# Kernel tuning notes

Hardware: AMD Instinct MI355X
Metric: run time of the kernel (lower is better)

## Reference

```python
import jax, jax.numpy as jnp
import numpy as np

E = 16          # expert_num
T = 8192        # token_num
H = 1024        # hidden_size
I = 4096        # intermediate_size
LN_EPS = 1e-12


def setup_inputs() -> dict:
    key = jax.random.key(0)
    ks = jax.random.split(key, 6)
    hidden_states = jax.random.normal(ks[0], (T, H), dtype=jnp.float32)
    perm = jax.random.permutation(ks[1], T).astype(jnp.int32)
    s1 = 1.0 / np.sqrt(H)
    s2 = 1.0 / np.sqrt(I)
    w1 = jax.random.uniform(ks[2], (E, I, H), jnp.float32, -s1, s1)
    b1 = jax.random.uniform(ks[3], (E, I), jnp.float32, -s1, s1)
    w2 = jax.random.uniform(ks[4], (E, H, I), jnp.float32, -s2, s2)
    b2 = jax.random.uniform(ks[5], (E, H), jnp.float32, -s2, s2)
    ln_gamma = jnp.ones((H,), jnp.float32)
    ln_beta = jnp.zeros((H,), jnp.float32)
    return {"hidden_states": hidden_states, "perm": perm, "w1": w1, "b1": b1,
            "w2": w2, "b2": b2, "ln_gamma": ln_gamma, "ln_beta": ln_beta}


def _layer_norm(x, gamma, beta, eps):
    mu = jnp.mean(x, axis=-1, keepdims=True)
    var = jnp.var(x, axis=-1, keepdims=True)
    return (x - mu) * jax.lax.rsqrt(var + eps) * gamma + beta


def reference(hidden_states, perm, w1, b1, w2, b2, ln_gamma, ln_beta):
    # dispatch: gather tokens by random permutation, group per expert
    xp = hidden_states[perm].reshape(E, T // E, H)            # [E, T/E, H]
    # grouped expert FFN (batched GEMM replaces the per-expert Python loop)
    h = jnp.einsum('eth,eih->eti', xp, w1) + b1[:, None, :]   # [E, T/E, I]
    h = jax.nn.gelu(h, approximate=False)
    o = jnp.einsum('eti,ehi->eth', h, w2) + b2[:, None, :]    # [E, T/E, H]
    # scatter-restore via inverse permutation
    restore = jnp.argsort(perm)
    o = o.reshape(T, H)[restore]
    # dropout is identity (p=0, eval); residual + LayerNorm
    return _layer_norm(o + hidden_states, ln_gamma, ln_beta, LN_EPS)
```

## Files before the change

### kernel.cpp

```cpp
#include <hip/hip_runtime.h>
#include <hip/hip_bf16.h>
#include <stdint.h>

#define E_NUM 16
#define T_NUM 8192
#define H_DIM 1024
#define I_DIM 4096
#define MPE   512

typedef __attribute__((ext_vector_type(8))) short short8;
typedef __attribute__((ext_vector_type(4))) float f32x4;
using bf16 = __hip_bfloat16;

typedef const __attribute__((address_space(1))) void GLV;
typedef __attribute__((address_space(3))) void LDSV;

__device__ __forceinline__ uint32_t pack2_bf16(float a, float b) {
  union { float f; uint32_t u; } ua, ub;
  ua.f = a; ub.f = b;
  uint32_t x = ua.u + (0x7FFFu + ((ua.u >> 16) & 1u));
  uint32_t y = ub.u + (0x7FFFu + ((ub.u >> 16) & 1u));
  return (x >> 16) | (y & 0xFFFF0000u);
}

__device__ __forceinline__ uint2 cvt4u(float4 a) {
  union { uint2 u; __hip_bfloat162 h[2]; } r;
  r.h[0] = __float22bfloat162_rn({a.x, a.y});
  r.h[1] = __float22bfloat162_rn({a.z, a.w});
  return r.u;
}

__device__ __forceinline__ float fast_gelu(float x) {
  const float p = x * fmaf(x * x, -0.0713548162726f, -1.59576912161f);
  return x * __builtin_amdgcn_rcpf(1.0f + __expf(p));
}

__global__ __launch_bounds__(256)
void gather_cast_kernel(const float* __restrict__ hs, const int* __restrict__ perm,
                        uint32_t* __restrict__ xp) {
  const int r = blockIdx.x;
  const int t = threadIdx.x;
  const int src = perm[r];
  float4 v = ((const float4*)(hs + (size_t)src * H_DIM))[t];
  uint2 o;
  o.x = pack2_bf16(v.x, v.y);
  o.y = pack2_bf16(v.z, v.w);
  ((uint2*)(xp + (size_t)r * (H_DIM / 2)))[t] = o;
}

template<int EPI, int KSPLIT, int N, int KFULL, int KLEN, int LOG_NBN>
__global__ __launch_bounds__(1024, 4)
void moe_gemm_kernel(const bf16* __restrict__ A, const float* __restrict__ Bw,
                     const float* __restrict__ bias, bf16* __restrict__ Hout,
                     float* __restrict__ Pout) {
  constexpr int NK = KLEN / 32;
  __shared__ bf16 As[2][512 * 32];
  __shared__ bf16 Bs[2][64 * 64];

  const int nwg = gridDim.x, qx = nwg >> 3, orig = blockIdx.x;
  const int wg = (orig & 7) * qx + (orig >> 3);
  const int bn   = wg & ((1 << LOG_NBN) - 1);
  const int rest = wg >> LOG_NBN;
  const int ks = (KSPLIT == 2) ? (rest & 1) : 0;
  const int e  = (KSPLIT == 2) ? (rest >> 1) : rest;
  const int K0 = ks * KLEN;

  const int tid = threadIdx.x;
  const int l = tid & 63;
  const int w = tid >> 6;
  const int wr = w >> 1, wc = w & 1;
  const int fr = l & 15, fq = l >> 4;
  const int rx = fr & 7;

  const bf16*  Ae = A  + (size_t)e * MPE * KFULL + K0;
  const float* Be = Bw + ((size_t)e * N + (size_t)bn * 128) * KFULL + K0;

  const int apq = tid >> 3;
  const int ag  = (tid & 7) ^ (apq & 7);
  const bf16* As0 = Ae + (size_t)(apq       + 256 * (ag >> 2)) * KFULL + (ag & 3) * 8;
  const bf16* As1 = Ae + (size_t)(apq + 128 + 256 * (ag >> 2)) * KFULL + (ag & 3) * 8;

  const int bc = tid >> 3, bsg = tid & 7;
  const float* Bsrc = Be + (size_t)bc * KFULL + bsg * 4;
  const int bp  = bc & 63;
  const int bwo = bp * 64 + (((((bc >> 6) << 2) | (bsg >> 1)) ^ (bp & 7)) << 3)
                + (bsg & 1) * 4;

  const int aso = (((((wr >> 2) << 2)) | fq) ^ rx) * 8;
  const int bro = fr * 64 + ((((wc << 2) | fq) ^ rx) << 3);

  f32x4 acc[4][4];
#pragma unroll
  for (int m = 0; m < 4; ++m)
#pragma unroll
    for (int n = 0; n < 4; ++n) acc[m][n] = (f32x4){0.f, 0.f, 0.f, 0.f};

  float4 breg;

#define ISSUE(buf, kt)                                                              \
  {                                                                                 \
    breg = *(const float4*)(Bsrc + (kt) * 32);                                      \
    __builtin_amdgcn_global_load_lds((GLV*)(As0 + (kt) * 32),                       \
                                     (LDSV*)&As[buf][tid * 8], 16, 0, 0);           \
    __builtin_amdgcn_global_load_lds((GLV*)(As1 + (kt) * 32),                       \
                                     (LDSV*)&As[buf][(1024 + tid) * 8], 16, 0, 0);  \
  }
#define WRITE_B(buf) { *(uint2*)&Bs[buf][bwo] = cvt4u(breg); }

  ISSUE(0, 0);
  asm volatile("s_waitcnt vmcnt(2)" ::: "memory");
  __builtin_amdgcn_sched_barrier(0);
  WRITE_B(0);
  asm volatile("s_waitcnt vmcnt(0) lgkmcnt(0)" ::: "memory");
  __builtin_amdgcn_sched_barrier(0);
  __builtin_amdgcn_s_barrier();
  __builtin_amdgcn_sched_barrier(0);

  for (int t = 0; t < NK; ++t) {
    const int cur = t & 1, nxt = cur ^ 1;
    const bool more = (t + 1) < NK;

    if (more) ISSUE(nxt, t + 1);

    short8 a8[4];
#pragma unroll
    for (int m = 0; m < 4; ++m)
      a8[m] = *(const short8*)&As[cur][((wr & 3) * 64 + m * 16 + fr) * 64 + aso];
    short8 b8[4];
#pragma unroll
    for (int n = 0; n < 4; ++n)
      b8[n] = *(const short8*)&Bs[cur][bro + n * 1024];
#pragma unroll
    for (int m = 0; m < 4; ++m)
#pragma unroll
      for (int n = 0; n < 4; ++n)
        acc[m][n] = __builtin_amdgcn_mfma_f32_16x16x32_bf16(a8[m], b8[n], acc[m][n], 0, 0, 0);

    if (more) {
      asm volatile("s_waitcnt vmcnt(2)" ::: "memory");
      __builtin_amdgcn_sched_barrier(0);
      WRITE_B(nxt);
      asm volatile("s_waitcnt vmcnt(0) lgkmcnt(0)" ::: "memory");
      __builtin_amdgcn_sched_barrier(0);
      __builtin_amdgcn_s_barrier();
      __builtin_amdgcn_sched_barrier(0);
    }
  }
#undef ISSUE
#undef WRITE_B
  __syncthreads();

  if (EPI == 1) {
    float bv[4];
#pragma unroll
    for (int n = 0; n < 4; ++n)
      bv[n] = bias[(size_t)e * N + bn * 128 + wc * 64 + n * 16 + fr];
    bf16* He = Hout + (size_t)e * MPE * N;

    bf16* Ls = &As[0][0];
#pragma unroll
    for (int P = 0; P < 2; ++P) {
      if ((wr >> 2) == P) {
        const int wrl = wr & 3;
#pragma unroll
        for (int m = 0; m < 4; ++m) {
#pragma unroll
          for (int j = 0; j < 4; ++j) {
            const int lr = wrl * 64 + m * 16 + fq * 4 + j;
#pragma unroll
            for (int n = 0; n < 4; ++n) {
              const int c = wc * 64 + n * 16 + fr;
              const int byteoff = lr * 256 + ((c * 2) ^ ((lr & 7) << 4));
              Ls[byteoff >> 1] = __float2bfloat16(fast_gelu(acc[m][n][j] + bv[n]));
            }
          }
        }
      }
      __syncthreads();
#pragma unroll
      for (int q = 0; q < 4; ++q) {
        const int o = (tid + q * 1024) * 16;
        const int lr = o >> 8;
        const int cb = o & 255;
        const int sb = lr * 256 + (cb ^ ((lr & 7) << 4));
        uint4 v = *(const uint4*)((const char*)Ls + sb);
        *(uint4*)&He[(size_t)(P * 256 + lr) * N + bn * 128 + (cb >> 1)] = v;
      }
      __syncthreads();
    }
  } else {
    float* Pd = Pout + (size_t)ks * T_NUM * H_DIM + (size_t)e * MPE * N;
#pragma unroll
    for (int m = 0; m < 4; ++m) {
#pragma unroll
      for (int j = 0; j < 4; ++j) {
        const int row = wr * 64 + m * 16 + fq * 4 + j;
#pragma unroll
        for (int n = 0; n < 4; ++n) {
          const int col = bn * 128 + wc * 64 + n * 16 + fr;
          Pd[(size_t)row * N + col] = acc[m][n][j];
        }
      }
    }
  }
}

__global__ __launch_bounds__(256)
void ln_resid2_kernel(float* __restrict__ out, const float* __restrict__ hs,
                      const float* __restrict__ p0, const float* __restrict__ p1,
                      const float* __restrict__ b2, const float* __restrict__ gamma,
                      const float* __restrict__ beta, const int* __restrict__ perm,
                      const int two) {
  const int r = blockIdx.x;
  const int t = threadIdx.x;
  const int e = r >> 9;
  const int drow = perm[r];
  float4 a = ((const float4*)(p0 + (size_t)r * H_DIM))[t];
  if (two) {
    float4 b = ((const float4*)(p1 + (size_t)r * H_DIM))[t];
    a.x += b.x; a.y += b.y; a.z += b.z; a.w += b.w;
  }
  float4 bb = ((const float4*)(b2 + (size_t)e * H_DIM))[t];
  float4 h  = ((const float4*)(hs + (size_t)drow * H_DIM))[t];
  float v0 = a.x + bb.x + h.x, v1 = a.y + bb.y + h.y;
  float v2 = a.z + bb.z + h.z, v3 = a.w + bb.w + h.w;
  float s  = v0 + v1 + v2 + v3;
  float sq = v0 * v0 + v1 * v1 + v2 * v2 + v3 * v3;
#pragma unroll
  for (int off = 32; off > 0; off >>= 1) {
    s  += __shfl_down(s, off);
    sq += __shfl_down(sq, off);
  }
  __shared__ float ss[4], ssq[4];
  const int wv = t >> 6;
  if ((t & 63) == 0) { ss[wv] = s; ssq[wv] = sq; }
  __syncthreads();
  s  = ss[0] + ss[1] + ss[2] + ss[3];
  sq = ssq[0] + ssq[1] + ssq[2] + ssq[3];
  const float mu  = s * (1.0f / (float)H_DIM);
  const float var = sq * (1.0f / (float)H_DIM) - mu * mu;
  const float rs  = rsqrtf(var + 1e-12f);
  float4 g = ((const float4*)gamma)[t];
  float4 b = ((const float4*)beta)[t];
  float4 rr;
  rr.x = (v0 - mu) * rs * g.x + b.x;
  rr.y = (v1 - mu) * rs * g.y + b.y;
  rr.z = (v2 - mu) * rs * g.z + b.z;
  rr.w = (v3 - mu) * rs * g.w + b.w;
  ((float4*)(out + (size_t)drow * H_DIM))[t] = rr;
}

extern "C" void kernel_launch(void* const* d_in, const int* in_sizes, int n_in,
                              void* d_out, int out_size, void* d_ws, size_t ws_size,
                              hipStream_t stream) {
  const float* hs    = (const float*)d_in[0];
  const int*   perm  = (const int*)d_in[1];
  const float* w1    = (const float*)d_in[2];
  const float* b1    = (const float*)d_in[3];
  const float* w2    = (const float*)d_in[4];
  const float* b2    = (const float*)d_in[5];
  const float* gamma = (const float*)d_in[6];
  const float* beta  = (const float*)d_in[7];
  float* out = (float*)d_out;

  const size_t xp_b   = (size_t)T_NUM * H_DIM * sizeof(bf16);
  const size_t hbuf_b = (size_t)T_NUM * I_DIM * sizeof(bf16);
  const size_t part_b = (size_t)T_NUM * H_DIM * sizeof(float);

  bf16*  xp   = (bf16*)d_ws;
  bf16*  hbuf = (bf16*)((char*)d_ws + xp_b);
  float* pbuf = (float*)((char*)d_ws + xp_b + hbuf_b);

  gather_cast_kernel<<<T_NUM, 256, 0, stream>>>(hs, perm, (uint32_t*)xp);

  moe_gemm_kernel<1, 1, I_DIM, H_DIM, H_DIM, 5>
      <<<512, 1024, 0, stream>>>(xp, w1, b1, hbuf, nullptr);

  if (ws_size >= xp_b + hbuf_b + 2 * part_b) {
    moe_gemm_kernel<0, 2, H_DIM, I_DIM, I_DIM / 2, 3>
        <<<256, 1024, 0, stream>>>(hbuf, w2, nullptr, nullptr, pbuf);
    ln_resid2_kernel<<<T_NUM, 256, 0, stream>>>(out, hs, pbuf, pbuf + (size_t)T_NUM * H_DIM,
                                                b2, gamma, beta, perm, 1);
  } else {
    moe_gemm_kernel<0, 1, H_DIM, I_DIM, I_DIM, 3>
        <<<128, 1024, 0, stream>>>(hbuf, w2, nullptr, nullptr, pbuf);
    ln_resid2_kernel<<<T_NUM, 256, 0, stream>>>(out, hs, pbuf, nullptr,
                                                b2, gamma, beta, perm, 0);
  }
}
```

Measured before the change: 293.8 us.

## Halve GEMM M-tile to 256 rows with 512-thread blocks

Splits each expert's 512-row M block into two 256-row tiles, so the grouped GEMMs use 512-thread workgroups and launch twice as many blocks. The A staging buffer shrinks and each thread now loads and converts eight fp32 weights per K-step instead of four. The aim is to cut per-workgroup LDS use and barrier cost and to raise parallelism and occupancy. In exchange, each fp32 weight tile is read and converted to bf16 twice as often, once per M half.

```diff
diff --git a/kernel.cpp b/kernel.cpp
--- a/kernel.cpp
+++ b/kernel.cpp
@@ -23,10 +23,12 @@
   return (x >> 16) | (y & 0xFFFF0000u);
 }
 
-__device__ __forceinline__ uint2 cvt4u(float4 a) {
-  union { uint2 u; __hip_bfloat162 h[2]; } r;
+__device__ __forceinline__ uint4 cvt8u(float4 a, float4 b) {
+  union { uint4 u; __hip_bfloat162 h[4]; } r;
   r.h[0] = __float22bfloat162_rn({a.x, a.y});
   r.h[1] = __float22bfloat162_rn({a.z, a.w});
+  r.h[2] = __float22bfloat162_rn({b.x, b.y});
+  r.h[3] = __float22bfloat162_rn({b.z, b.w});
   return r.u;
 }
 
@@ -49,18 +51,19 @@
 }
 
 template<int EPI, int KSPLIT, int N, int KFULL, int KLEN, int LOG_NBN>
-__global__ __launch_bounds__(1024, 4)
+__global__ __launch_bounds__(512, 2)
 void moe_gemm_kernel(const bf16* __restrict__ A, const float* __restrict__ Bw,
                      const float* __restrict__ bias, bf16* __restrict__ Hout,
                      float* __restrict__ Pout) {
   constexpr int NK = KLEN / 32;
-  __shared__ bf16 As[2][512 * 32];
+  __shared__ bf16 As[2][256 * 32];
   __shared__ bf16 Bs[2][64 * 64];
 
   const int nwg = gridDim.x, qx = nwg >> 3, orig = blockIdx.x;
   const int wg = (orig & 7) * qx + (orig >> 3);
-  const int bn   = wg & ((1 << LOG_NBN) - 1);
-  const int rest = wg >> LOG_NBN;
+  const int bm   = wg & 1;
+  const int bn   = (wg >> 1) & ((1 << LOG_NBN) - 1);
+  const int rest = wg >> (1 + LOG_NBN);
   const int ks = (KSPLIT == 2) ? (rest & 1) : 0;
   const int e  = (KSPLIT == 2) ? (rest >> 1) : rest;
   const int K0 = ks * KLEN;
@@ -72,21 +75,20 @@
   const int fr = l & 15, fq = l >> 4;
   const int rx = fr & 7;
 
-  const bf16*  Ae = A  + (size_t)e * MPE * KFULL + K0;
+  const bf16*  Ae = A  + ((size_t)e * MPE + (size_t)bm * 256) * KFULL + K0;
   const float* Be = Bw + ((size_t)e * N + (size_t)bn * 128) * KFULL + K0;
 
-  const int apq = tid >> 3;
-  const int ag  = (tid & 7) ^ (apq & 7);
-  const bf16* As0 = Ae + (size_t)(apq       + 256 * (ag >> 2)) * KFULL + (ag & 3) * 8;
-  const bf16* As1 = Ae + (size_t)(apq + 128 + 256 * (ag >> 2)) * KFULL + (ag & 3) * 8;
-
-  const int bc = tid >> 3, bsg = tid & 7;
-  const float* Bsrc = Be + (size_t)bc * KFULL + bsg * 4;
+  const int p0 = tid >> 3;
+  const int ga = (tid & 7) ^ (p0 & 7);
+  const bf16* As0 = Ae + (size_t)(p0      + 128 * (ga >> 2)) * KFULL + (ga & 3) * 8;
+  const bf16* As1 = Ae + (size_t)(p0 + 64 + 128 * (ga >> 2)) * KFULL + (ga & 3) * 8;
+
+  const int bc = tid >> 2, bsg = tid & 3;
+  const float* Bsrc = Be + (size_t)bc * KFULL + bsg * 8;
   const int bp  = bc & 63;
-  const int bwo = bp * 64 + (((((bc >> 6) << 2) | (bsg >> 1)) ^ (bp & 7)) << 3)
-                + (bsg & 1) * 4;
-
-  const int aso = (((((wr >> 2) << 2)) | fq) ^ rx) * 8;
+  const int bwo = bp * 64 + (((((bc >> 6) << 2) | bsg) ^ (bp & 7)) << 3);
+
+  const int aso = (((((wr >> 1) << 2)) | fq) ^ rx) * 8;
   const int bro = fr * 64 + ((((wc << 2) | fq) ^ rx) << 3);
 
   f32x4 acc[4][4];
@@ -95,17 +97,18 @@
 #pragma unroll
     for (int n = 0; n < 4; ++n) acc[m][n] = (f32x4){0.f, 0.f, 0.f, 0.f};
 
-  float4 breg;
+  float4 br0, br1;
 
 #define ISSUE(buf, kt)                                                              \
   {                                                                                 \
-    breg = *(const float4*)(Bsrc + (kt) * 32);                                      \
+    br0 = *(const float4*)(Bsrc + (kt) * 32);                                       \
+    br1 = *(const float4*)(Bsrc + (kt) * 32 + 4);                                   \
     __builtin_amdgcn_global_load_lds((GLV*)(As0 + (kt) * 32),                       \
                                      (LDSV*)&As[buf][tid * 8], 16, 0, 0);           \
     __builtin_amdgcn_global_load_lds((GLV*)(As1 + (kt) * 32),                       \
-                                     (LDSV*)&As[buf][(1024 + tid) * 8], 16, 0, 0);  \
-  }
-#define WRITE_B(buf) { *(uint2*)&Bs[buf][bwo] = cvt4u(breg); }
+                                     (LDSV*)&As[buf][(512 + tid) * 8], 16, 0, 0);   \
+  }
+#define WRITE_B(buf) { *(uint4*)&Bs[buf][bwo] = cvt8u(br0, br1); }
 
   ISSUE(0, 0);
   asm volatile("s_waitcnt vmcnt(2)" ::: "memory");
@@ -125,7 +128,7 @@
     short8 a8[4];
 #pragma unroll
     for (int m = 0; m < 4; ++m)
-      a8[m] = *(const short8*)&As[cur][((wr & 3) * 64 + m * 16 + fr) * 64 + aso];
+      a8[m] = *(const short8*)&As[cur][((wr & 1) * 64 + m * 16 + fr) * 64 + aso];
     short8 b8[4];
 #pragma unroll
     for (int n = 0; n < 4; ++n)
@@ -160,8 +163,8 @@
     bf16* Ls = &As[0][0];
 #pragma unroll
     for (int P = 0; P < 2; ++P) {
-      if ((wr >> 2) == P) {
-        const int wrl = wr & 3;
+      if ((wr >> 1) == P) {
+        const int wrl = wr & 1;
 #pragma unroll
         for (int m = 0; m < 4; ++m) {
 #pragma unroll
@@ -179,12 +182,12 @@
       __syncthreads();
 #pragma unroll
       for (int q = 0; q < 4; ++q) {
-        const int o = (tid + q * 1024) * 16;
+        const int o = (tid + q * 512) * 16;
         const int lr = o >> 8;
         const int cb = o & 255;
         const int sb = lr * 256 + (cb ^ ((lr & 7) << 4));
         uint4 v = *(const uint4*)((const char*)Ls + sb);
-        *(uint4*)&He[(size_t)(P * 256 + lr) * N + bn * 128 + (cb >> 1)] = v;
+        *(uint4*)&He[(size_t)(bm * 256 + P * 128 + lr) * N + bn * 128 + (cb >> 1)] = v;
       }
       __syncthreads();
     }
@@ -194,7 +197,7 @@
     for (int m = 0; m < 4; ++m) {
 #pragma unroll
       for (int j = 0; j < 4; ++j) {
-        const int row = wr * 64 + m * 16 + fq * 4 + j;
+        const int row = bm * 256 + wr * 64 + m * 16 + fq * 4 + j;
 #pragma unroll
         for (int n = 0; n < 4; ++n) {
           const int col = bn * 128 + wc * 64 + n * 16 + fr;
@@ -274,16 +277,16 @@
   gather_cast_kernel<<<T_NUM, 256, 0, stream>>>(hs, perm, (uint32_t*)xp);
 
   moe_gemm_kernel<1, 1, I_DIM, H_DIM, H_DIM, 5>
-      <<<512, 1024, 0, stream>>>(xp, w1, b1, hbuf, nullptr);
+      <<<1024, 512, 0, stream>>>(xp, w1, b1, hbuf, nullptr);
 
   if (ws_size >= xp_b + hbuf_b + 2 * part_b) {
     moe_gemm_kernel<0, 2, H_DIM, I_DIM, I_DIM / 2, 3>
-        <<<256, 1024, 0, stream>>>(hbuf, w2, nullptr, nullptr, pbuf);
+        <<<512, 512, 0, stream>>>(hbuf, w2, nullptr, nullptr, pbuf);
     ln_resid2_kernel<<<T_NUM, 256, 0, stream>>>(out, hs, pbuf, pbuf + (size_t)T_NUM * H_DIM,
                                                 b2, gamma, beta, perm, 1);
   } else {
     moe_gemm_kernel<0, 1, H_DIM, I_DIM, I_DIM, 3>
-        <<<128, 1024, 0, stream>>>(hbuf, w2, nullptr, nullptr, pbuf);
+        <<<256, 512, 0, stream>>>(hbuf, w2, nullptr, nullptr, pbuf);
     ln_resid2_kernel<<<T_NUM, 256, 0, stream>>>(out, hs, pbuf, nullptr,
                                                 b2, gamma, beta, perm, 0);
   }
```

Result: faster. 275.6 us (median of 2 runs) (-6.2%).
